# Kernel tuning notes

Hardware: AMD Instinct MI355X
Metric: run time of the kernel (lower is better)

Reference implementation:

```python
import jax, jax.numpy as jnp
import numpy as np

N = 50000      # nodes
E = 800000     # edges (avg degree 16)
D = 64         # num_node_features
H = 64         # hidden_channels
G = 512        # graphs in batch
OUT = 32       # final linear output
NEG_SLOPE = 0.2


def setup_inputs() -> dict:
    key = jax.random.key(0)
    ks = jax.random.split(key, 20)
    s = 0.1  # param init scale
    inp = {
        "x": jax.random.normal(ks[0], (N, D), jnp.float32),
        "edge_index": jax.random.randint(ks[1], (2, E), 0, N, dtype=jnp.int64),
        "batch": jnp.sort(jax.random.randint(ks[2], (N,), 0, G, dtype=jnp.int64)),
        # GATv2 layer 1 (D -> H)
        "Wl1": jax.random.normal(ks[3], (D, H), jnp.float32) * s,
        "bl1": jnp.zeros((H,), jnp.float32),
        "Wr1": jax.random.normal(ks[4], (D, H), jnp.float32) * s,
        "br1": jnp.zeros((H,), jnp.float32),
        "att1": jax.random.normal(ks[5], (H,), jnp.float32) * s,
        "bias1": jnp.zeros((H,), jnp.float32),
        # GATv2 layer 2 (H -> H)
        "Wl2": jax.random.normal(ks[6], (H, H), jnp.float32) * s,
        "bl2": jnp.zeros((H,), jnp.float32),
        "Wr2": jax.random.normal(ks[7], (H, H), jnp.float32) * s,
        "br2": jnp.zeros((H,), jnp.float32),
        "att2": jax.random.normal(ks[8], (H,), jnp.float32) * s,
        "bias2": jnp.zeros((H,), jnp.float32),
        # final classifier
        "lin_w": jax.random.normal(ks[9], (H, OUT), jnp.float32) * s,
        "lin_b": jnp.zeros((OUT,), jnp.float32),
    }
    return inp


def _gatv2(x, src, dst, Wl, bl, Wr, br, att, bias):
    # GATv2Conv, heads=1, PyG semantics: messages flow src -> dst
    xl = x @ Wl + bl                       # [N, H] source transform (also the message)
    xr = x @ Wr + br                       # [N, H] destination transform
    z = xl[src] + xr[dst]                  # [E, H] gather
    e = jax.nn.leaky_relu(z, NEG_SLOPE) @ att  # [E] edge scores
    # segment softmax over edges grouped by destination node
    m = jax.ops.segment_max(e, dst, num_segments=N)   # [N]
    ex = jnp.exp(e - m[dst])                          # [E]
    denom = jax.ops.segment_sum(ex, dst, num_segments=N)  # [N]
    alpha = ex / denom[dst]                            # [E]
    out = jax.ops.segment_sum(alpha[:, None] * xl[src], dst, num_segments=N)  # [N, H]
    return out + bias


def reference(x, edge_index, batch,
              Wl1, bl1, Wr1, br1, att1, bias1,
              Wl2, bl2, Wr2, br2, att2, bias2,
              lin_w, lin_b):
    src, dst = edge_index[0], edge_index[1]
    h = jax.nn.relu(_gatv2(x, src, dst, Wl1, bl1, Wr1, br1, att1, bias1))
    h = jax.nn.relu(_gatv2(h, src, dst, Wl2, bl2, Wr2, br2, att2, bias2))
    # global mean pool over graphs
    sums = jax.ops.segment_sum(h, batch, num_segments=G)          # [G, H]
    cnts = jax.ops.segment_sum(jnp.ones((h.shape[0],), h.dtype), batch, num_segments=G)
    pooled = sums / jnp.maximum(cnts, 1.0)[:, None]
    # dropout(p=0.5) is identity at inference
    return pooled @ lin_w + lin_b                                  # [G, 32]
```

## Files before the change

### kernel.cpp

```cpp
#include <hip/hip_runtime.h>
#include <hip/hip_fp16.h>
#include <math.h>


#define ELLC    48
#define OVF_CAP 65536
#define ECHUNK  2048

typedef int      vint4 __attribute__((ext_vector_type(4)));
typedef _Float16 half4 __attribute__((ext_vector_type(4)));

#define GROWS 32
template <typename T>
__device__ __forceinline__ void dual_gemm_slim(
    int bid, int t,
    const T* __restrict__ X,
    const float* __restrict__ Wl, const float* __restrict__ bl,
    const float* __restrict__ Wr, const float* __restrict__ br,
    _Float16* __restrict__ xl, _Float16* __restrict__ xr, int n,
    float* xS) {
    int row0 = bid * GROWS;
    for (int i = t; i < GROWS * 16; i += 256) {
        int r = row0 + (i >> 4);
        float4 v = make_float4(0.f, 0.f, 0.f, 0.f);
        if (r < n) {
            if constexpr (sizeof(T) == 2) {
                half4 hv = ((const half4*)(X + (size_t)r * 64))[i & 15];
                v = make_float4((float)hv[0], (float)hv[1], (float)hv[2], (float)hv[3]);
            } else {
                v = ((const float4*)(X + (size_t)r * 64))[i & 15];
            }
        }
        ((float4*)xS)[i] = v;
    }
    __syncthreads();
    int h  = t & 63;
    int rb = t >> 6;
    float accl[8], accr[8];
#pragma unroll
    for (int i = 0; i < 8; ++i) { accl[i] = 0.f; accr[i] = 0.f; }
#pragma unroll 4
    for (int d = 0; d < 64; ++d) {
        float wl = Wl[d * 64 + h];
        float wr = Wr[d * 64 + h];
#pragma unroll
        for (int i = 0; i < 8; ++i) {
            float xv = xS[(rb + 4 * i) * 64 + d];
            accl[i] += xv * wl;
            accr[i] += xv * wr;
        }
    }
    float blv = bl[h], brv = br[h];
#pragma unroll
    for (int i = 0; i < 8; ++i) {
        int r = row0 + rb + 4 * i;
        if (r < n) {
            xl[(size_t)r * 64 + h] = (_Float16)(accl[i] + blv);
            xr[(size_t)r * 64 + h] = (_Float16)(accr[i] + brv);
        }
    }
    __syncthreads();
}

__global__ __launch_bounds__(256) void dual_gemm64_f16_kernel(
    const _Float16* __restrict__ X,
    const float* __restrict__ Wl, const float* __restrict__ bl,
    const float* __restrict__ Wr, const float* __restrict__ br,
    _Float16* __restrict__ xl, _Float16* __restrict__ xr, int n) {
    __shared__ float xS[GROWS * 64];
    dual_gemm_slim<_Float16>(blockIdx.x, threadIdx.x, X, Wl, bl, Wr, br,
                             xl, xr, n, xS);
}

__global__ __launch_bounds__(256) void fill_gemm_kernel(
    const int* __restrict__ src, const int* __restrict__ dst,
    int* __restrict__ cnt, unsigned short* __restrict__ ell,
    int* __restrict__ novf, int* __restrict__ ovf_dst, int* __restrict__ ovf_src,
    int E, int N, int psize, int fb, int ggrid,
    const float* __restrict__ X,
    const float* __restrict__ Wl, const float* __restrict__ bl,
    const float* __restrict__ Wr, const float* __restrict__ br,
    _Float16* __restrict__ xl, _Float16* __restrict__ xr) {
    __shared__ float xS[GROWS * 64];
    int b = blockIdx.x;
    int q = b / 16, r = b % 16;
    if (r >= 8) {
        int vg = q * 8 + (r - 8);
        if (vg < ggrid)
            dual_gemm_slim<float>(vg, threadIdx.x, X, Wl, bl, Wr, br,
                                  xl, xr, N, xS);
        return;
    }
    int vb = q * 8 + r;
    if (vb >= fb) return;
    int t     = threadIdx.x;
    int chunk = vb >> 2;
    int p     = vb & 3;
    int d0    = p * psize;
    int d1    = min(N, d0 + psize);
    int e0    = chunk * ECHUNK;
    int e1    = min(E, e0 + ECHUNK);
    int nq    = (e1 - e0) >> 2;
    const vint4* dst4 = (const vint4*)(dst + e0);
    const vint4* src4 = (const vint4*)(src + e0);

    auto scatter4 = [&](vint4 dv, vint4 sv) {
#pragma unroll
        for (int k = 0; k < 4; ++k) {
            int d = dv[k];
            int s = sv[k];
            if (d >= d0 && d < d1) {
                int pos = atomicAdd(&cnt[d], 1);
                if (pos < ELLC) {
                    ell[d * ELLC + pos] = (unsigned short)s;
                } else {
                    int j = atomicAdd(novf, 1);
                    if (j < OVF_CAP) { ovf_dst[j] = d; ovf_src[j] = s; }
                }
            }
        }
    };

    if (nq == (ECHUNK >> 2)) {
        vint4 dvA = __builtin_nontemporal_load(&dst4[t]);
        vint4 svA = __builtin_nontemporal_load(&src4[t]);
        vint4 dvB = __builtin_nontemporal_load(&dst4[t + 256]);
        vint4 svB = __builtin_nontemporal_load(&src4[t + 256]);
        scatter4(dvA, svA);
        scatter4(dvB, svB);
    } else {
        for (int qq = t; qq < nq; qq += 256) {
            vint4 dv = __builtin_nontemporal_load(&dst4[qq]);
            vint4 sv = __builtin_nontemporal_load(&src4[qq]);
            scatter4(dv, sv);
        }
        for (int e = e0 + (nq << 2) + t; e < e1; e += 256) {
            int d = dst[e];
            if (d >= d0 && d < d1) {
                int pos = atomicAdd(&cnt[d], 1);
                int s   = src[e];
                if (pos < ELLC) {
                    ell[d * ELLC + pos] = (unsigned short)s;
                } else {
                    int j = atomicAdd(novf, 1);
                    if (j < OVF_CAP) { ovf_dst[j] = d; ovf_src[j] = s; }
                }
            }
        }
    }
}

__global__ __launch_bounds__(256) void gat_aggregate_kernel(
    const _Float16* __restrict__ xl, const _Float16* __restrict__ xr,
    const int* __restrict__ cnt, const unsigned short* __restrict__ ell,
    const int* __restrict__ novf, const int* __restrict__ ovf_dst,
    const int* __restrict__ ovf_src,
    const float* __restrict__ att, const float* __restrict__ bias,
    _Float16* __restrict__ out, int n) {
    int wid  = (blockIdx.x * blockDim.x + threadIdx.x) >> 6;
    int lane = threadIdx.x & 63;
    if (wid >= n) return;
    int g = lane >> 4;
    int l = lane & 15;
    int d = wid;

    float4 att4 = ((const float4*)att)[l];
    float4 b4   = ((const float4*)bias)[l];
    int deg_d = cnt[d];
    int nd  = min(deg_d, ELLC);
    int beg = d * ELLC;

    float  s   = 0.f;
    float4 acc = make_float4(0.f, 0.f, 0.f, 0.f);

    if (deg_d > 0) {
        int myidx = 0;
        if (lane < ELLC) myidx = (int)ell[beg + lane];
        int i_first = __shfl(myidx, 0);

        half4 xrh = ((const half4*)(xr + (size_t)d * 64))[l];
        float4 xr4 = make_float4((float)xrh[0], (float)xrh[1], (float)xrh[2], (float)xrh[3]);

#pragma unroll 6
        for (int k = 0; k * 8 < nd; ++k) {
            int  sa = k * 8 + g, sb = sa + 4;
            bool aa = sa < nd,   ab = sb < nd;
            int  i0 = __shfl(myidx, sa); if (!aa) i0 = i_first;
            int  i1 = __shfl(myidx, sb); if (!ab) i1 = i_first;
            half4 h0 = ((const half4*)(xl + (size_t)i0 * 64))[l];
            half4 h1 = ((const half4*)(xl + (size_t)i1 * 64))[l];
            float4 x0 = make_float4((float)h0[0], (float)h0[1], (float)h0[2], (float)h0[3]);
            float4 x1 = make_float4((float)h1[0], (float)h1[1], (float)h1[2], (float)h1[3]);
            float z, c0 = 0.f, c1 = 0.f;
            z = x0.x + xr4.x; c0 += ((z > 0.f) ? z : 0.2f * z) * att4.x;
            z = x0.y + xr4.y; c0 += ((z > 0.f) ? z : 0.2f * z) * att4.y;
            z = x0.z + xr4.z; c0 += ((z > 0.f) ? z : 0.2f * z) * att4.z;
            z = x0.w + xr4.w; c0 += ((z > 0.f) ? z : 0.2f * z) * att4.w;
            z = x1.x + xr4.x; c1 += ((z > 0.f) ? z : 0.2f * z) * att4.x;
            z = x1.y + xr4.y; c1 += ((z > 0.f) ? z : 0.2f * z) * att4.y;
            z = x1.z + xr4.z; c1 += ((z > 0.f) ? z : 0.2f * z) * att4.z;
            z = x1.w + xr4.w; c1 += ((z > 0.f) ? z : 0.2f * z) * att4.w;
#pragma unroll
            for (int sh = 8; sh >= 1; sh >>= 1) {
                c0 += __shfl_xor(c0, sh);
                c1 += __shfl_xor(c1, sh);
            }
            float w0 = aa ? __expf(fminf(c0, 30.f)) : 0.f;
            float w1 = ab ? __expf(fminf(c1, 30.f)) : 0.f;
            s += w0 + w1;
            acc.x += w0 * x0.x + w1 * x1.x;
            acc.y += w0 * x0.y + w1 * x1.y;
            acc.z += w0 * x0.z + w1 * x1.z;
            acc.w += w0 * x0.w + w1 * x1.w;
        }
        if (deg_d > ELLC) {
            int no = min(*novf, OVF_CAP);
            for (int j = g; j < no; j += 4) {
                bool active = (ovf_dst[j] == d);
                int  i0     = active ? ovf_src[j] : i_first;
                half4 h0 = ((const half4*)(xl + (size_t)i0 * 64))[l];
                float4 x0 = make_float4((float)h0[0], (float)h0[1], (float)h0[2], (float)h0[3]);
                float z, c0 = 0.f;
                z = x0.x + xr4.x; c0 += ((z > 0.f) ? z : 0.2f * z) * att4.x;
                z = x0.y + xr4.y; c0 += ((z > 0.f) ? z : 0.2f * z) * att4.y;
                z = x0.z + xr4.z; c0 += ((z > 0.f) ? z : 0.2f * z) * att4.z;
                z = x0.w + xr4.w; c0 += ((z > 0.f) ? z : 0.2f * z) * att4.w;
#pragma unroll
                for (int sh = 8; sh >= 1; sh >>= 1) c0 += __shfl_xor(c0, sh);
                float w0 = active ? __expf(fminf(c0, 30.f)) : 0.f;
                s += w0;
                acc.x += w0 * x0.x;
                acc.y += w0 * x0.y;
                acc.z += w0 * x0.z;
                acc.w += w0 * x0.w;
            }
        }
#pragma unroll
        for (int mask = 16; mask <= 32; mask <<= 1) {
            s     += __shfl_xor(s, mask);
            acc.x += __shfl_xor(acc.x, mask);
            acc.y += __shfl_xor(acc.y, mask);
            acc.z += __shfl_xor(acc.z, mask);
            acc.w += __shfl_xor(acc.w, mask);
        }
    }
    if (g == 0) {
        float inv = (s > 0.f) ? (1.f / s) : 0.f;
        half4 hv;
        hv[0] = (_Float16)fmaxf(acc.x * inv + b4.x, 0.f);
        hv[1] = (_Float16)fmaxf(acc.y * inv + b4.y, 0.f);
        hv[2] = (_Float16)fmaxf(acc.z * inv + b4.z, 0.f);
        hv[3] = (_Float16)fmaxf(acc.w * inv + b4.w, 0.f);
        ((half4*)(out + (size_t)d * 64))[l] = hv;
    }
}

__global__ __launch_bounds__(256) void pool_final_kernel(
    const _Float16* __restrict__ h, const int* __restrict__ batch,
    const float* __restrict__ lin_w, const float* __restrict__ lin_b,
    float* __restrict__ out, int N, int G) {
    int g = blockIdx.x;
    int t = threadIdx.x;
    auto lb = [&](int key) {
        int lo = 0, hi = N;
        while (lo < hi) {
            int mid = (lo + hi) >> 1;
            if (batch[mid] < key) lo = mid + 1; else hi = mid;
        }
        return lo;
    };
    int start = lb(g), end = lb(g + 1);

    __shared__ float part[4][64];
    __shared__ float pooled[64];
    int f = t & 63, w = t >> 6;
    float acc = 0.f;
    for (int i = start + w; i < end; i += 4)
        acc += (float)h[(size_t)i * 64 + f];
    part[w][f] = acc;
    __syncthreads();
    if (t < 64) {
        float s = part[0][t] + part[1][t] + part[2][t] + part[3][t];
        pooled[t] = s / fmaxf((float)(end - start), 1.f);
    }
    __syncthreads();
    if (t < 32) {
        float a = 0.f;
#pragma unroll 8
        for (int hh = 0; hh < 64; ++hh) a += pooled[hh] * lin_w[hh * 32 + t];
        out[g * 32 + t] = a + lin_b[t];
    }
}

extern "C" void kernel_launch(void* const* d_in, const int* in_sizes, int n_in,
                              void* d_out, int out_size, void* d_ws, size_t ws_size,
                              hipStream_t stream) {
    const float* x     = (const float*)d_in[0];
    const int*   ei    = (const int*)d_in[1];
    const int*   batch = (const int*)d_in[2];
    const float* Wl1   = (const float*)d_in[3];
    const float* bl1   = (const float*)d_in[4];
    const float* Wr1   = (const float*)d_in[5];
    const float* br1   = (const float*)d_in[6];
    const float* att1  = (const float*)d_in[7];
    const float* bias1 = (const float*)d_in[8];
    const float* Wl2   = (const float*)d_in[9];
    const float* bl2   = (const float*)d_in[10];
    const float* Wr2   = (const float*)d_in[11];
    const float* br2   = (const float*)d_in[12];
    const float* att2  = (const float*)d_in[13];
    const float* bias2 = (const float*)d_in[14];
    const float* lin_w = (const float*)d_in[15];
    const float* lin_b = (const float*)d_in[16];
    float* out = (float*)d_out;

    const int N = in_sizes[0] / 64;
    const int E = in_sizes[1] / 2;
    const int G = out_size / 32;
    const int* src = ei;
    const int* dst = ei + E;

    char*  ws  = (char*)d_ws;
    size_t off = 0;
    auto alloc = [&](size_t bytes) -> void* {
        void* p = ws + off;
        off += bytes;
        off = (off + 255) & ~(size_t)255;
        return p;
    };
    _Float16* xl   = (_Float16*)alloc((size_t)N * 64 * sizeof(_Float16));
    _Float16* xr   = (_Float16*)alloc((size_t)N * 64 * sizeof(_Float16));
    _Float16* h1   = (_Float16*)alloc((size_t)N * 64 * sizeof(_Float16));
    int*   cnt     = (int*)alloc((size_t)N * sizeof(int));
    int*   novf    = (int*)alloc(256);
    char*  zend    = ws + off;
    unsigned short* ell = (unsigned short*)alloc((size_t)N * ELLC * sizeof(unsigned short));
    int*   ovf_dst = (int*)alloc((size_t)OVF_CAP * sizeof(int));
    int*   ovf_src = (int*)alloc((size_t)OVF_CAP * sizeof(int));

    (void)hipMemsetAsync(cnt, 0, (size_t)(zend - (char*)cnt), stream);

    int ggrid  = (N + GROWS - 1) / GROWS;
    int agrid  = (N + 3) / 4;
    int nchunk = (E + ECHUNK - 1) / ECHUNK;
    int fb     = nchunk * 4;
    int psize  = (N + 3) / 4;
    int ngroups = max((fb + 7) / 8, (ggrid + 7) / 8);
    int igrid   = ngroups * 16;

    fill_gemm_kernel<<<igrid, 256, 0, stream>>>(
        src, dst, cnt, ell, novf, ovf_dst, ovf_src, E, N, psize, fb, ggrid,
        x, Wl1, bl1, Wr1, br1, xl, xr);

    gat_aggregate_kernel<<<agrid, 256, 0, stream>>>(
        xl, xr, cnt, ell, novf, ovf_dst, ovf_src, att1, bias1, h1, N);

    dual_gemm64_f16_kernel<<<ggrid, 256, 0, stream>>>(
        h1, Wl2, bl2, Wr2, br2, xl, xr, N);

    gat_aggregate_kernel<<<agrid, 256, 0, stream>>>(
        xl, xr, cnt, ell, novf, ovf_dst, ovf_src, att2, bias2, h1, N);

    pool_final_kernel<<<G, 256, 0, stream>>>(h1, batch, lin_w, lin_b, out, N, G);
}
```

Baseline: 245.7 us.

## Process two destination nodes per wavefront in GAT aggregation; store xr in fp32

The aggregate kernel now assigns two destination nodes to each 64-lane wavefront and interleaves four independent neighbor gathers per iteration, halving the grid. This is meant to raise memory-level parallelism and amortize per-wave setup. The destination transform xr is also kept in fp32, which removes the half-to-float conversion but doubles its storage and read traffic. Nodes with different degrees share one loop bounded by the larger degree, so some lanes do masked work, and register pressure rises.

Result: slower. 253.6 us (+3.2%).

```diff
diff --git a/kernel.cpp b/kernel.cpp
--- a/kernel.cpp
+++ b/kernel.cpp
@@ -17,7 +17,7 @@
     const T* __restrict__ X,
     const float* __restrict__ Wl, const float* __restrict__ bl,
     const float* __restrict__ Wr, const float* __restrict__ br,
-    _Float16* __restrict__ xl, _Float16* __restrict__ xr, int n,
+    _Float16* __restrict__ xl, float* __restrict__ xr, int n,
     float* xS) {
     int row0 = bid * GROWS;
     for (int i = t; i < GROWS * 16; i += 256) {
@@ -56,7 +56,7 @@
         int r = row0 + rb + 4 * i;
         if (r < n) {
             xl[(size_t)r * 64 + h] = (_Float16)(accl[i] + blv);
-            xr[(size_t)r * 64 + h] = (_Float16)(accr[i] + brv);
+            xr[(size_t)r * 64 + h] = accr[i] + brv;
         }
     }
     __syncthreads();
@@ -66,7 +66,7 @@
     const _Float16* __restrict__ X,
     const float* __restrict__ Wl, const float* __restrict__ bl,
     const float* __restrict__ Wr, const float* __restrict__ br,
-    _Float16* __restrict__ xl, _Float16* __restrict__ xr, int n) {
+    _Float16* __restrict__ xl, float* __restrict__ xr, int n) {
     __shared__ float xS[GROWS * 64];
     dual_gemm_slim<_Float16>(blockIdx.x, threadIdx.x, X, Wl, bl, Wr, br,
                              xl, xr, n, xS);
@@ -80,7 +80,7 @@
     const float* __restrict__ X,
     const float* __restrict__ Wl, const float* __restrict__ bl,
     const float* __restrict__ Wr, const float* __restrict__ br,
-    _Float16* __restrict__ xl, _Float16* __restrict__ xr) {
+    _Float16* __restrict__ xl, float* __restrict__ xr) {
     __shared__ float xS[GROWS * 64];
     int b = blockIdx.x;
     int q = b / 16, r = b % 16;
@@ -151,7 +151,7 @@
 }
 
 __global__ __launch_bounds__(256) void gat_aggregate_kernel(
-    const _Float16* __restrict__ xl, const _Float16* __restrict__ xr,
+    const _Float16* __restrict__ xl, const float* __restrict__ xr,
     const int* __restrict__ cnt, const unsigned short* __restrict__ ell,
     const int* __restrict__ novf, const int* __restrict__ ovf_dst,
     const int* __restrict__ ovf_src,
@@ -159,99 +159,150 @@
     _Float16* __restrict__ out, int n) {
     int wid  = (blockIdx.x * blockDim.x + threadIdx.x) >> 6;
     int lane = threadIdx.x & 63;
-    if (wid >= n) return;
+    int d0 = wid * 2, d1 = d0 + 1;
+    if (d0 >= n) return;
+    bool has1 = (d1 < n);
     int g = lane >> 4;
     int l = lane & 15;
-    int d = wid;
 
     float4 att4 = ((const float4*)att)[l];
     float4 b4   = ((const float4*)bias)[l];
-    int deg_d = cnt[d];
-    int nd  = min(deg_d, ELLC);
-    int beg = d * ELLC;
-
-    float  s   = 0.f;
-    float4 acc = make_float4(0.f, 0.f, 0.f, 0.f);
-
-    if (deg_d > 0) {
-        int myidx = 0;
-        if (lane < ELLC) myidx = (int)ell[beg + lane];
-        int i_first = __shfl(myidx, 0);
-
-        half4 xrh = ((const half4*)(xr + (size_t)d * 64))[l];
-        float4 xr4 = make_float4((float)xrh[0], (float)xrh[1], (float)xrh[2], (float)xrh[3]);
+    int deg0 = cnt[d0];
+    int deg1 = has1 ? cnt[d1] : 0;
+    int nd0 = min(deg0, ELLC), nd1 = min(deg1, ELLC);
+
+    int my0 = 0, my1 = 0;
+    if (lane < ELLC) {
+        my0 = (int)ell[d0 * ELLC + lane];
+        if (has1) my1 = (int)ell[d1 * ELLC + lane];
+    }
+    int f0 = (deg0 > 0) ? __shfl(my0, 0) : 0;
+    int f1 = (deg1 > 0) ? __shfl(my1, 0) : 0;
+
+    float4 xr40 = ((const float4*)(xr + (size_t)d0 * 64))[l];
+    float4 xr41 = has1 ? ((const float4*)(xr + (size_t)d1 * 64))[l]
+                       : make_float4(0.f, 0.f, 0.f, 0.f);
+
+    float  s0 = 0.f, s1 = 0.f;
+    float4 a0 = make_float4(0.f, 0.f, 0.f, 0.f);
+    float4 a1 = make_float4(0.f, 0.f, 0.f, 0.f);
+    int ndmax = max(nd0, nd1);
 
 #pragma unroll 6
-        for (int k = 0; k * 8 < nd; ++k) {
-            int  sa = k * 8 + g, sb = sa + 4;
-            bool aa = sa < nd,   ab = sb < nd;
-            int  i0 = __shfl(myidx, sa); if (!aa) i0 = i_first;
-            int  i1 = __shfl(myidx, sb); if (!ab) i1 = i_first;
+    for (int k = 0; k * 8 < ndmax; ++k) {
+        int  sa  = k * 8 + g, sb = sa + 4;
+        bool a00 = sa < nd0, a01 = sb < nd0;
+        bool a10 = sa < nd1, a11 = sb < nd1;
+        int i00 = __shfl(my0, sa); if (!a00) i00 = f0;
+        int i01 = __shfl(my0, sb); if (!a01) i01 = f0;
+        int i10 = __shfl(my1, sa); if (!a10) i10 = f1;
+        int i11 = __shfl(my1, sb); if (!a11) i11 = f1;
+        half4 h00 = ((const half4*)(xl + (size_t)i00 * 64))[l];
+        half4 h01 = ((const half4*)(xl + (size_t)i01 * 64))[l];
+        half4 h10 = ((const half4*)(xl + (size_t)i10 * 64))[l];
+        half4 h11 = ((const half4*)(xl + (size_t)i11 * 64))[l];
+        float4 x00 = make_float4((float)h00[0], (float)h00[1], (float)h00[2], (float)h00[3]);
+        float4 x01 = make_float4((float)h01[0], (float)h01[1], (float)h01[2], (float)h01[3]);
+        float4 x10 = make_float4((float)h10[0], (float)h10[1], (float)h10[2], (float)h10[3]);
+        float4 x11 = make_float4((float)h11[0], (float)h11[1], (float)h11[2], (float)h11[3]);
+        float z, c00 = 0.f, c01 = 0.f, c10 = 0.f, c11 = 0.f;
+        z = x00.x + xr40.x; c00 += ((z > 0.f) ? z : 0.2f * z) * att4.x;
+        z = x00.y + xr40.y; c00 += ((z > 0.f) ? z : 0.2f * z) * att4.y;
+        z = x00.z + xr40.z; c00 += ((z > 0.f) ? z : 0.2f * z) * att4.z;
+        z = x00.w + xr40.w; c00 += ((z > 0.f) ? z : 0.2f * z) * att4.w;
+        z = x01.x + xr40.x; c01 += ((z > 0.f) ? z : 0.2f * z) * att4.x;
+        z = x01.y + xr40.y; c01 += ((z > 0.f) ? z : 0.2f * z) * att4.y;
+        z = x01.z + xr40.z; c01 += ((z > 0.f) ? z : 0.2f * z) * att4.z;
+        z = x01.w + xr40.w; c01 += ((z > 0.f) ? z : 0.2f * z) * att4.w;
+        z = x10.x + xr41.x; c10 += ((z > 0.f) ? z : 0.2f * z) * att4.x;
+        z = x10.y + xr41.y; c10 += ((z > 0.f) ? z : 0.2f * z) * att4.y;
+        z = x10.z + xr41.z; c10 += ((z > 0.f) ? z : 0.2f * z) * att4.z;
+        z = x10.w + xr41.w; c10 += ((z > 0.f) ? z : 0.2f * z) * att4.w;
+        z = x11.x + xr41.x; c11 += ((z > 0.f) ? z : 0.2f * z) * att4.x;
+        z = x11.y + xr41.y; c11 += ((z > 0.f) ? z : 0.2f * z) * att4.y;
+        z = x11.z + xr41.z; c11 += ((z > 0.f) ? z : 0.2f * z) * att4.z;
+        z = x11.w + xr41.w; c11 += ((z > 0.f) ? z : 0.2f * z) * att4.w;
+#pragma unroll
+        for (int sh = 8; sh >= 1; sh >>= 1) {
+            c00 += __shfl_xor(c00, sh);
+            c01 += __shfl_xor(c01, sh);
+            c10 += __shfl_xor(c10, sh);
+            c11 += __shfl_xor(c11, sh);
+        }
+        float w00 = a00 ? __expf(fminf(c00, 30.f)) : 0.f;
+        float w01 = a01 ? __expf(fminf(c01, 30.f)) : 0.f;
+        float w10 = a10 ? __expf(fminf(c10, 30.f)) : 0.f;
+        float w11 = a11 ? __expf(fminf(c11, 30.f)) : 0.f;
+        s0 += w00 + w01;
+        s1 += w10 + w11;
+        a0.x += w00 * x00.x + w01 * x01.x;
+        a0.y += w00 * x00.y + w01 * x01.y;
+        a0.z += w00 * x00.z + w01 * x01.z;
+        a0.w += w00 * x00.w + w01 * x01.w;
+        a1.x += w10 * x10.x + w11 * x11.x;
+        a1.y += w10 * x10.y + w11 * x11.y;
+        a1.z += w10 * x10.z + w11 * x11.z;
+        a1.w += w10 * x10.w + w11 * x11.w;
+    }
+    if (deg0 > ELLC || deg1 > ELLC) {
+        int no = min(*novf, OVF_CAP);
+        for (int j = g; j < no; j += 4) {
+            int od = ovf_dst[j];
+            bool m0 = (od == d0), m1 = (od == d1);
+            if (!(m0 || m1)) continue;
+            int  i0 = ovf_src[j];
             half4 h0 = ((const half4*)(xl + (size_t)i0 * 64))[l];
-            half4 h1 = ((const half4*)(xl + (size_t)i1 * 64))[l];
             float4 x0 = make_float4((float)h0[0], (float)h0[1], (float)h0[2], (float)h0[3]);
-            float4 x1 = make_float4((float)h1[0], (float)h1[1], (float)h1[2], (float)h1[3]);
-            float z, c0 = 0.f, c1 = 0.f;
-            z = x0.x + xr4.x; c0 += ((z > 0.f) ? z : 0.2f * z) * att4.x;
-            z = x0.y + xr4.y; c0 += ((z > 0.f) ? z : 0.2f * z) * att4.y;
-            z = x0.z + xr4.z; c0 += ((z > 0.f) ? z : 0.2f * z) * att4.z;
-            z = x0.w + xr4.w; c0 += ((z > 0.f) ? z : 0.2f * z) * att4.w;
-            z = x1.x + xr4.x; c1 += ((z > 0.f) ? z : 0.2f * z) * att4.x;
-            z = x1.y + xr4.y; c1 += ((z > 0.f) ? z : 0.2f * z) * att4.y;
-            z = x1.z + xr4.z; c1 += ((z > 0.f) ? z : 0.2f * z) * att4.z;
-            z = x1.w + xr4.w; c1 += ((z > 0.f) ? z : 0.2f * z) * att4.w;
-#pragma unroll
-            for (int sh = 8; sh >= 1; sh >>= 1) {
-                c0 += __shfl_xor(c0, sh);
-                c1 += __shfl_xor(c1, sh);
+            float4 xrr = m0 ? xr40 : xr41;
+            float z, c0 = 0.f;
+            z = x0.x + xrr.x; c0 += ((z > 0.f) ? z : 0.2f * z) * att4.x;
+            z = x0.y + xrr.y; c0 += ((z > 0.f) ? z : 0.2f * z) * att4.y;
+            z = x0.z + xrr.z; c0 += ((z > 0.f) ? z : 0.2f * z) * att4.z;
+            z = x0.w + xrr.w; c0 += ((z > 0.f) ? z : 0.2f * z) * att4.w;
+#pragma unroll
+            for (int sh = 8; sh >= 1; sh >>= 1) c0 += __shfl_xor(c0, sh);
+            float w0 = __expf(fminf(c0, 30.f));
+            if (m0) {
+                s0 += w0;
+                a0.x += w0 * x0.x; a0.y += w0 * x0.y;
+                a0.z += w0 * x0.z; a0.w += w0 * x0.w;
+            } else {
+                s1 += w0;
+                a1.x += w0 * x0.x; a1.y += w0 * x0.y;
+                a1.z += w0 * x0.z; a1.w += w0 * x0.w;
             }
-            float w0 = aa ? __expf(fminf(c0, 30.f)) : 0.f;
-            float w1 = ab ? __expf(fminf(c1, 30.f)) : 0.f;
-            s += w0 + w1;
-            acc.x += w0 * x0.x + w1 * x1.x;
-            acc.y += w0 * x0.y + w1 * x1.y;
-            acc.z += w0 * x0.z + w1 * x1.z;
-            acc.w += w0 * x0.w + w1 * x1.w;
-        }
-        if (deg_d > ELLC) {
-            int no = min(*novf, OVF_CAP);
-            for (int j = g; j < no; j += 4) {
-                bool active = (ovf_dst[j] == d);
-                int  i0     = active ? ovf_src[j] : i_first;
-                half4 h0 = ((const half4*)(xl + (size_t)i0 * 64))[l];
-                float4 x0 = make_float4((float)h0[0], (float)h0[1], (float)h0[2], (float)h0[3]);
-                float z, c0 = 0.f;
-                z = x0.x + xr4.x; c0 += ((z > 0.f) ? z : 0.2f * z) * att4.x;
-                z = x0.y + xr4.y; c0 += ((z > 0.f) ? z : 0.2f * z) * att4.y;
-                z = x0.z + xr4.z; c0 += ((z > 0.f) ? z : 0.2f * z) * att4.z;
-                z = x0.w + xr4.w; c0 += ((z > 0.f) ? z : 0.2f * z) * att4.w;
-#pragma unroll
-                for (int sh = 8; sh >= 1; sh >>= 1) c0 += __shfl_xor(c0, sh);
-                float w0 = active ? __expf(fminf(c0, 30.f)) : 0.f;
-                s += w0;
-                acc.x += w0 * x0.x;
-                acc.y += w0 * x0.y;
-                acc.z += w0 * x0.z;
-                acc.w += w0 * x0.w;
-            }
-        }
-#pragma unroll
-        for (int mask = 16; mask <= 32; mask <<= 1) {
-            s     += __shfl_xor(s, mask);
-            acc.x += __shfl_xor(acc.x, mask);
-            acc.y += __shfl_xor(acc.y, mask);
-            acc.z += __shfl_xor(acc.z, mask);
-            acc.w += __shfl_xor(acc.w, mask);
-        }
+        }
+    }
+#pragma unroll
+    for (int mask = 16; mask <= 32; mask <<= 1) {
+        s0   += __shfl_xor(s0, mask);
+        s1   += __shfl_xor(s1, mask);
+        a0.x += __shfl_xor(a0.x, mask);
+        a0.y += __shfl_xor(a0.y, mask);
+        a0.z += __shfl_xor(a0.z, mask);
+        a0.w += __shfl_xor(a0.w, mask);
+        a1.x += __shfl_xor(a1.x, mask);
+        a1.y += __shfl_xor(a1.y, mask);
+        a1.z += __shfl_xor(a1.z, mask);
+        a1.w += __shfl_xor(a1.w, mask);
     }
     if (g == 0) {
-        float inv = (s > 0.f) ? (1.f / s) : 0.f;
+        float inv0 = (s0 > 0.f) ? (1.f / s0) : 0.f;
         half4 hv;
-        hv[0] = (_Float16)fmaxf(acc.x * inv + b4.x, 0.f);
-        hv[1] = (_Float16)fmaxf(acc.y * inv + b4.y, 0.f);
-        hv[2] = (_Float16)fmaxf(acc.z * inv + b4.z, 0.f);
-        hv[3] = (_Float16)fmaxf(acc.w * inv + b4.w, 0.f);
-        ((half4*)(out + (size_t)d * 64))[l] = hv;
+        hv[0] = (_Float16)fmaxf(a0.x * inv0 + b4.x, 0.f);
+        hv[1] = (_Float16)fmaxf(a0.y * inv0 + b4.y, 0.f);
+        hv[2] = (_Float16)fmaxf(a0.z * inv0 + b4.z, 0.f);
+        hv[3] = (_Float16)fmaxf(a0.w * inv0 + b4.w, 0.f);
+        ((half4*)(out + (size_t)d0 * 64))[l] = hv;
+        if (has1) {
+            float inv1 = (s1 > 0.f) ? (1.f / s1) : 0.f;
+            half4 hw;
+            hw[0] = (_Float16)fmaxf(a1.x * inv1 + b4.x, 0.f);
+            hw[1] = (_Float16)fmaxf(a1.y * inv1 + b4.y, 0.f);
+            hw[2] = (_Float16)fmaxf(a1.z * inv1 + b4.z, 0.f);
+            hw[3] = (_Float16)fmaxf(a1.w * inv1 + b4.w, 0.f);
+            ((half4*)(out + (size_t)d1 * 64))[l] = hw;
+        }
     }
 }
 
@@ -329,7 +380,7 @@
         return p;
     };
     _Float16* xl   = (_Float16*)alloc((size_t)N * 64 * sizeof(_Float16));
-    _Float16* xr   = (_Float16*)alloc((size_t)N * 64 * sizeof(_Float16));
+    float* xr      = (float*)alloc((size_t)N * 64 * sizeof(float));
     _Float16* h1   = (_Float16*)alloc((size_t)N * 64 * sizeof(_Float16));
     int*   cnt     = (int*)alloc((size_t)N * sizeof(int));
     int*   novf    = (int*)alloc(256);
@@ -341,7 +392,7 @@
     (void)hipMemsetAsync(cnt, 0, (size_t)(zend - (char*)cnt), stream);
 
     int ggrid  = (N + GROWS - 1) / GROWS;
-    int agrid  = (N + 3) / 4;
+    int agrid  = (N + 7) / 8;
     int nchunk = (E + ECHUNK - 1) / ECHUNK;
     int fb     = nchunk * 4;
     int psize  = (N + 3) / 4;
```
